# Optimization experiments

Measured on AMD Instinct MI355X. Metric: run time of the kernel, lower is better.

Reference implementation:

```python
import jax, jax.numpy as jnp
import numpy as np

N = 100000
E = 1600000
IN_DIM = 128
OUT_DIM = 128


def setup_inputs() -> dict:
    key = jax.random.key(0)
    k1, k2, k3, k4, k5 = jax.random.split(key, 5)
    x = jax.random.normal(k1, (N, IN_DIM), dtype=jnp.float32)
    edge_index = jax.random.randint(k2, (2, E), 0, N, dtype=jnp.int64)
    # LayerNorm affine params
    ln_w = jnp.ones((IN_DIM,), dtype=jnp.float32)
    ln_b = jnp.zeros((IN_DIM,), dtype=jnp.float32)
    # SAGEConv params: lin_l (neighbor agg, with bias), lin_r (root, no bias)
    s = 1.0 / np.sqrt(IN_DIM)
    W_l = jax.random.uniform(k3, (OUT_DIM, IN_DIM), dtype=jnp.float32, minval=-s, maxval=s)
    b_l = jax.random.uniform(k4, (OUT_DIM,), dtype=jnp.float32, minval=-s, maxval=s)
    W_r = jax.random.uniform(k5, (OUT_DIM, IN_DIM), dtype=jnp.float32, minval=-s, maxval=s)
    return {"x": x, "edge_index": edge_index, "ln_w": ln_w, "ln_b": ln_b,
            "W_l": W_l, "b_l": b_l, "W_r": W_r}


def _layer_norm(x, w, b, eps=1e-5):
    mu = jnp.mean(x, axis=-1, keepdims=True)
    var = jnp.mean(jnp.square(x - mu), axis=-1, keepdims=True)
    return (x - mu) * jax.lax.rsqrt(var + eps) * w + b


def reference(x, edge_index, ln_w, ln_b, W_l, b_l, W_r):
    # norm -> activation -> dropout(p=0, identity)
    h = jax.nn.relu(_layer_norm(x, ln_w, ln_b))  # [N, in_dim]
    src = edge_index[0]  # message sources (x_j)
    dst = edge_index[1]  # aggregation targets
    # mean aggregation of neighbor features onto target nodes
    agg = jax.ops.segment_sum(h[src], dst, num_segments=N)  # [N, in_dim]
    cnt = jax.ops.segment_sum(jnp.ones((E,), dtype=h.dtype), dst, num_segments=N)
    agg = agg / jnp.maximum(cnt, 1.0)[:, None]
    # SAGEConv: lin_l(agg) + lin_r(h)
    out = agg @ W_l.T + b_l + h @ W_r.T  # [N, out_dim]
    return out
```

## Files before the change

kernel.cpp:

```cpp
#include <hip/hip_runtime.h>

#define N_NODES 100000
#define E_EDGES 1600000
#define DIM     128

#define NB1     391
#define NBINS   512
#define NBH     (NBINS * NB1)
#define HS_BLOCKS 196

#define HB_OFF    0
#define WTB_OFF   25600000
#define OFFS_OFF  25665536
#define BH_OFF    26065600
#define BSUM_OFF  26868416
#define BIN_OFF   26869440
#define SRC_OFF   33269440

typedef __attribute__((ext_vector_type(8))) short short8;
typedef __attribute__((ext_vector_type(4))) float floatx4;

__device__ __forceinline__ unsigned bf16pack(float a, float b) {
  unsigned ua = __float_as_uint(a); ua += 0x7fffu + ((ua >> 16) & 1u);
  unsigned ub = __float_as_uint(b); ub += 0x7fffu + ((ub >> 16) & 1u);
  return (ua >> 16) | (ub & 0xffff0000u);
}
__device__ __forceinline__ float2 bf16unpack(unsigned p) {
  return make_float2(__uint_as_float(p << 16), __uint_as_float(p & 0xffff0000u));
}

__global__ __launch_bounds__(256) void k_prep(const float* __restrict__ x,
                                              const float* __restrict__ lw,
                                              const float* __restrict__ lb,
                                              const float* __restrict__ Wl,
                                              const float* __restrict__ Wr,
                                              const int* __restrict__ ei,
                                              unsigned* __restrict__ hb,
                                              unsigned* __restrict__ wtb,
                                              int* __restrict__ bh) {
  int gid = blockIdx.x * 256 + threadIdx.x;
  int t = threadIdx.x;

  {
    int row  = blockIdx.x * 4 + (t >> 6);
    int lane = t & 63;
    float2 v = ((const float2*)(x + (size_t)row * DIM))[lane];
    float s  = v.x + v.y;
    float sq = v.x * v.x + v.y * v.y;
    #pragma unroll
    for (int off = 32; off > 0; off >>= 1) {
      s  += __shfl_xor(s, off);
      sq += __shfl_xor(sq, off);
    }
    float mu  = s * (1.0f / 128.0f);
    float var = sq * (1.0f / 128.0f) - mu * mu;
    float rs  = rsqrtf(var + 1e-5f);
    float2 w = ((const float2*)lw)[lane];
    float2 b = ((const float2*)lb)[lane];
    float ox = fmaxf((v.x - mu) * rs * w.x + b.x, 0.0f);
    float oy = fmaxf((v.y - mu) * rs * w.y + b.y, 0.0f);
    hb[(size_t)row * 64 + lane] = bf16pack(ox, oy);
  }

  if (gid < 16384) {
    int j2 = gid & 3;
    int q  = (gid >> 2) & 3;
    int c  = (gid >> 4) & 127;
    int kb = gid >> 11;
    int k0 = kb * 32 + q * 8 + j2 * 2;
    int k1 = k0 + 1;
    float v0 = (k0 < 128) ? Wl[c * 128 + k0] : Wr[c * 128 + (k0 - 128)];
    float v1 = (k1 < 128) ? Wl[c * 128 + k1] : Wr[c * 128 + (k1 - 128)];
    wtb[gid] = bf16pack(v0, v1);
  }

  if (blockIdx.x < NB1) {
    __shared__ int h[NBINS];
    h[t] = 0; h[t + 256] = 0;
    __syncthreads();
    const int4* d4p = (const int4*)(ei + E_EDGES);
    #pragma unroll
    for (int u = 0; u < 4; ++u) {
      int i4 = blockIdx.x * 1024 + u * 256 + t;
      if (i4 < E_EDGES / 4) {
        int4 d = d4p[i4];
        atomicAdd(&h[d.x >> 8], 1);
        atomicAdd(&h[d.y >> 8], 1);
        atomicAdd(&h[d.z >> 8], 1);
        atomicAdd(&h[d.w >> 8], 1);
      }
    }
    __syncthreads();
    bh[t * NB1 + blockIdx.x] = h[t];
    bh[(t + 256) * NB1 + blockIdx.x] = h[t + 256];
  }
}

__global__ __launch_bounds__(256) void k_hscan1(int* __restrict__ bh,
                                                int* __restrict__ bsum) {
  __shared__ int s[256];
  int t = threadIdx.x;
  int base = blockIdx.x * 1024 + t * 4;
  int a0 = (base + 0 < NBH) ? bh[base + 0] : 0;
  int a1 = (base + 1 < NBH) ? bh[base + 1] : 0;
  int a2 = (base + 2 < NBH) ? bh[base + 2] : 0;
  int a3 = (base + 3 < NBH) ? bh[base + 3] : 0;
  s[t] = a0 + a1 + a2 + a3;
  __syncthreads();
  #pragma unroll
  for (int off = 1; off < 256; off <<= 1) {
    int x = (t >= off) ? s[t - off] : 0;
    __syncthreads();
    s[t] += x;
    __syncthreads();
  }
  int excl = (t > 0) ? s[t - 1] : 0;
  if (t == 255) bsum[blockIdx.x] = s[255];
  if (base + 0 < NBH) bh[base + 0] = excl;
  if (base + 1 < NBH) bh[base + 1] = excl + a0;
  if (base + 2 < NBH) bh[base + 2] = excl + a0 + a1;
  if (base + 3 < NBH) bh[base + 3] = excl + a0 + a1 + a2;
}

__global__ __launch_bounds__(256) void k_hscan2(int* __restrict__ bh,
                                                const int* __restrict__ bsum) {
  __shared__ int s[256];
  int t = threadIdx.x;
  s[t] = (t < HS_BLOCKS) ? bsum[t] : 0;
  __syncthreads();
  #pragma unroll
  for (int off = 1; off < 256; off <<= 1) {
    int x = (t >= off) ? s[t - off] : 0;
    __syncthreads();
    s[t] += x;
    __syncthreads();
  }
  int blk = blockIdx.x;
  int add = (blk > 0) ? s[blk - 1] : 0;
  #pragma unroll
  for (int u = 0; u < 4; ++u) {
    int i = blk * 1024 + t * 4 + u;
    if (i < NBH) bh[i] += add;
  }
}

__global__ __launch_bounds__(256) void k_scatter1(const int* __restrict__ ei,
                                                  const int* __restrict__ bh,
                                                  int* __restrict__ binned) {
  __shared__ int cur[NBINS];
  int t = threadIdx.x;
  cur[t] = bh[t * NB1 + blockIdx.x];
  cur[t + 256] = bh[(t + 256) * NB1 + blockIdx.x];
  __syncthreads();
  const int4* s4p = (const int4*)ei;
  const int4* d4p = (const int4*)(ei + E_EDGES);
  #pragma unroll
  for (int u = 0; u < 4; ++u) {
    int i4 = blockIdx.x * 1024 + u * 256 + t;
    if (i4 < E_EDGES / 4) {
      int4 sv = s4p[i4];
      int4 dv = d4p[i4];
      int p0 = atomicAdd(&cur[dv.x >> 8], 1);
      int p1 = atomicAdd(&cur[dv.y >> 8], 1);
      int p2 = atomicAdd(&cur[dv.z >> 8], 1);
      int p3 = atomicAdd(&cur[dv.w >> 8], 1);
      binned[p0] = sv.x | ((dv.x & 255) << 20);
      binned[p1] = sv.y | ((dv.y & 255) << 20);
      binned[p2] = sv.z | ((dv.z & 255) << 20);
      binned[p3] = sv.w | ((dv.w & 255) << 20);
    }
  }
}

__global__ __launch_bounds__(256) void k_csr(const int* __restrict__ bh,
                                             const int* __restrict__ binned,
                                             int* __restrict__ offs,
                                             int* __restrict__ srcidx) {
  __shared__ int h[256];
  __shared__ int s[256];
  __shared__ int cur[256];
  int t = threadIdx.x;
  int bin = blockIdx.x;
  int base = bh[bin * NB1];
  int end  = bh[(bin + 1) * NB1];
  h[t] = 0;
  __syncthreads();
  for (int i = base + t; i < end; i += 256)
    atomicAdd(&h[(binned[i] >> 20) & 255], 1);
  __syncthreads();
  s[t] = h[t];
  __syncthreads();
  #pragma unroll
  for (int off = 1; off < 256; off <<= 1) {
    int x = (t >= off) ? s[t - off] : 0;
    __syncthreads();
    s[t] += x;
    __syncthreads();
  }
  int excl = (t > 0) ? s[t - 1] : 0;
  cur[t] = excl;
  int node = bin * 256 + t;
  if (node < N_NODES) offs[node] = base + excl;
  if (node == N_NODES) offs[N_NODES] = E_EDGES;
  __syncthreads();
  for (int i = base + t; i < end; i += 256) {
    int p = binned[i];
    int r = atomicAdd(&cur[(p >> 20) & 255], 1);
    srcidx[base + r] = p & 0xFFFFF;
  }
}

__global__ __launch_bounds__(512) void k_gathgemm(const unsigned* __restrict__ hb,
                                                  const int* __restrict__ offs,
                                                  const int* __restrict__ srcidx,
                                                  const unsigned* __restrict__ wtb,
                                                  const float* __restrict__ bl,
                                                  float* __restrict__ out) {
  __shared__ unsigned agg[16 * 68];
  int wv   = threadIdx.x >> 6;
  int lane = threadIdx.x & 63;
  int r0 = blockIdx.x * 16;
  int n0 = r0 + wv * 2;
  int n1 = n0 + 1;
  int b0 = __builtin_amdgcn_readfirstlane(offs[n0]);
  int e0 = __builtin_amdgcn_readfirstlane(offs[n0 + 1]);
  int b1 = __builtin_amdgcn_readfirstlane(offs[n1]);
  int e1 = __builtin_amdgcn_readfirstlane(offs[n1 + 1]);
  int m0 = e0 - b0, m1 = e1 - b1;
  int c  = (m0 < m1 ? m0 : m1) & ~7;

  float ax0 = 0.0f, ay0 = 0.0f, ax1 = 0.0f, ay1 = 0.0f;

  for (int j = 0; j < c; j += 8) {
    unsigned p0[8], p1[8];
    #pragma unroll
    for (int i = 0; i < 8; ++i) {
      int s0 = srcidx[b0 + j + i];
      int s1 = srcidx[b1 + j + i];
      p0[i] = hb[(size_t)s0 * 64 + lane];
      p1[i] = hb[(size_t)s1 * 64 + lane];
    }
    #pragma unroll
    for (int i = 0; i < 8; ++i) {
      float2 v0 = bf16unpack(p0[i]);
      float2 v1 = bf16unpack(p1[i]);
      ax0 += v0.x; ay0 += v0.y;
      ax1 += v1.x; ay1 += v1.y;
    }
  }
  for (int j = b0 + c; j < e0; ) {
    int rem = e0 - j;
    if (rem >= 8) {
      unsigned p[8];
      #pragma unroll
      for (int i = 0; i < 8; ++i) p[i] = hb[(size_t)srcidx[j + i] * 64 + lane];
      #pragma unroll
      for (int i = 0; i < 8; ++i) { float2 v = bf16unpack(p[i]); ax0 += v.x; ay0 += v.y; }
      j += 8;
    } else {
      float2 v = bf16unpack(hb[(size_t)srcidx[j] * 64 + lane]);
      ax0 += v.x; ay0 += v.y;
      ++j;
    }
  }
  for (int j = b1 + c; j < e1; ) {
    int rem = e1 - j;
    if (rem >= 8) {
      unsigned p[8];
      #pragma unroll
      for (int i = 0; i < 8; ++i) p[i] = hb[(size_t)srcidx[j + i] * 64 + lane];
      #pragma unroll
      for (int i = 0; i < 8; ++i) { float2 v = bf16unpack(p[i]); ax1 += v.x; ay1 += v.y; }
      j += 8;
    } else {
      float2 v = bf16unpack(hb[(size_t)srcidx[j] * 64 + lane]);
      ax1 += v.x; ay1 += v.y;
      ++j;
    }
  }

  float inv0 = 1.0f / fmaxf((float)m0, 1.0f);
  float inv1 = 1.0f / fmaxf((float)m1, 1.0f);
  agg[(wv * 2 + 0) * 68 + lane] = bf16pack(ax0 * inv0, ay0 * inv0);
  agg[(wv * 2 + 1) * 68 + lane] = bf16pack(ax1 * inv1, ay1 * inv1);
  __syncthreads();

  int m = lane & 15;
  int q = lane >> 4;
  int rowA = r0 + m;

  short8 afrag[8];
  #pragma unroll
  for (int kb = 0; kb < 4; ++kb) {
    uint4 u = *(const uint4*)&agg[m * 68 + (kb * 4 + q) * 4];
    afrag[kb] = *(short8*)&u;
  }
  const uint4* hr = (const uint4*)(hb + (size_t)rowA * 64);
  #pragma unroll
  for (int kb = 0; kb < 4; ++kb) {
    uint4 u = hr[kb * 4 + q];
    afrag[kb + 4] = *(short8*)&u;
  }

  const uint4* b4 = (const uint4*)wtb;
  int ct = wv;
  int col = ct * 16 + m;
  floatx4 acc = {0.0f, 0.0f, 0.0f, 0.0f};
  #pragma unroll
  for (int kb = 0; kb < 8; ++kb) {
    uint4 u = b4[kb * 512 + col * 4 + q];
    short8 bfrag = *(short8*)&u;
    acc = __builtin_amdgcn_mfma_f32_16x16x32_bf16(afrag[kb], bfrag, acc, 0, 0, 0);
  }
  float bias = bl[col];
  #pragma unroll
  for (int reg = 0; reg < 4; ++reg) {
    int r = r0 + q * 4 + reg;
    out[(size_t)r * DIM + col] = acc[reg] + bias;
  }
}

extern "C" void kernel_launch(void* const* d_in, const int* in_sizes, int n_in,
                              void* d_out, int out_size, void* d_ws, size_t ws_size,
                              hipStream_t stream) {
  const float* x  = (const float*)d_in[0];
  const int*   ei = (const int*)d_in[1];
  const float* lw = (const float*)d_in[2];
  const float* lb = (const float*)d_in[3];
  const float* Wl = (const float*)d_in[4];
  const float* bl = (const float*)d_in[5];
  const float* Wr = (const float*)d_in[6];
  float* out = (float*)d_out;

  char* ws = (char*)d_ws;
  unsigned* hb     = (unsigned*)(ws + HB_OFF);
  unsigned* wtb    = (unsigned*)(ws + WTB_OFF);
  int*      offs   = (int*)(ws + OFFS_OFF);
  int*      bh     = (int*)(ws + BH_OFF);
  int*      bsum   = (int*)(ws + BSUM_OFF);
  int*      binned = (int*)(ws + BIN_OFF);
  int*      srcidx = (int*)(ws + SRC_OFF);

  k_prep<<<N_NODES / 4, 256, 0, stream>>>(x, lw, lb, Wl, Wr, ei, hb, wtb, bh);
  k_hscan1<<<HS_BLOCKS, 256, 0, stream>>>(bh, bsum);
  k_hscan2<<<HS_BLOCKS, 256, 0, stream>>>(bh, bsum);
  k_scatter1<<<NB1, 256, 0, stream>>>(ei, bh, binned);
  k_csr<<<NB1, 256, 0, stream>>>(bh, binned, offs, srcidx);
  k_gathgemm<<<N_NODES / 16, 512, 0, stream>>>(hb, offs, srcidx, wtb, bl, out);
}
```

Measured before the change: 261.7 us.

## Stage edge binning in shared memory before coalesced scatter to global

The bin-scatter kernel now processes 8192-edge chunks per block. Each block builds a local histogram and scan, places the packed edges into a shared-memory staging buffer ordered by bin, and then writes them out linearly, so global stores from each bin land in contiguous runs instead of random addresses. The chunk size doubles, which halves the number of per-block histogram columns and scan blocks, and the CSR launch count is decoupled from the chunk count. The cost is an extra histogram pass, about 64KB of LDS per block, and fewer blocks, which may lower occupancy.

```diff
diff --git a/kernel.cpp b/kernel.cpp
--- a/kernel.cpp
+++ b/kernel.cpp
@@ -4,18 +4,20 @@
 #define E_EDGES 1600000
 #define DIM     128
 
-#define NB1     391
+#define NB1     196
+#define CHUNK   8192
 #define NBINS   512
+#define NBUCKET 391
 #define NBH     (NBINS * NB1)
-#define HS_BLOCKS 196
+#define HS_BLOCKS 98
 
 #define HB_OFF    0
 #define WTB_OFF   25600000
 #define OFFS_OFF  25665536
 #define BH_OFF    26065600
-#define BSUM_OFF  26868416
-#define BIN_OFF   26869440
-#define SRC_OFF   33269440
+#define BSUM_OFF  26467008
+#define BIN_OFF   26468032
+#define SRC_OFF   32868032
 
 typedef __attribute__((ext_vector_type(8))) short short8;
 typedef __attribute__((ext_vector_type(4))) float floatx4;
@@ -80,8 +82,8 @@
     __syncthreads();
     const int4* d4p = (const int4*)(ei + E_EDGES);
     #pragma unroll
-    for (int u = 0; u < 4; ++u) {
-      int i4 = blockIdx.x * 1024 + u * 256 + t;
+    for (int u = 0; u < 8; ++u) {
+      int i4 = blockIdx.x * (CHUNK / 4) + u * 256 + t;
       if (i4 < E_EDGES / 4) {
         int4 d = d4p[i4];
         atomicAdd(&h[d.x >> 8], 1);
@@ -144,32 +146,92 @@
   }
 }
 
-__global__ __launch_bounds__(256) void k_scatter1(const int* __restrict__ ei,
-                                                  const int* __restrict__ bh,
-                                                  int* __restrict__ binned) {
+__global__ __launch_bounds__(256) void k_binsort(const int* __restrict__ ei,
+                                                 const int* __restrict__ bh,
+                                                 int* __restrict__ binned) {
+  __shared__ int stage[CHUNK];
+  __shared__ int addr[CHUNK];
+  __shared__ int hist[NBINS];
+  __shared__ int ebase[NBINS];
   __shared__ int cur[NBINS];
-  int t = threadIdx.x;
-  cur[t] = bh[t * NB1 + blockIdx.x];
-  cur[t + 256] = bh[(t + 256) * NB1 + blockIdx.x];
-  __syncthreads();
+  __shared__ int gbase[NBINS];
+  __shared__ int s[256];
+  int t  = threadIdx.x;
+  int ch = blockIdx.x;
+
+  hist[t] = 0; hist[t + 256] = 0;
+  gbase[t] = bh[t * NB1 + ch];
+  gbase[t + 256] = bh[(t + 256) * NB1 + ch];
+  __syncthreads();
+
   const int4* s4p = (const int4*)ei;
   const int4* d4p = (const int4*)(ei + E_EDGES);
-  #pragma unroll
-  for (int u = 0; u < 4; ++u) {
-    int i4 = blockIdx.x * 1024 + u * 256 + t;
+
+  #pragma unroll
+  for (int u = 0; u < 8; ++u) {
+    int i4 = ch * (CHUNK / 4) + u * 256 + t;
+    if (i4 < E_EDGES / 4) {
+      int4 d = d4p[i4];
+      atomicAdd(&hist[d.x >> 8], 1);
+      atomicAdd(&hist[d.y >> 8], 1);
+      atomicAdd(&hist[d.z >> 8], 1);
+      atomicAdd(&hist[d.w >> 8], 1);
+    }
+  }
+  __syncthreads();
+
+  int h0 = hist[2 * t], h1 = hist[2 * t + 1];
+  s[t] = h0 + h1;
+  __syncthreads();
+  #pragma unroll
+  for (int off = 1; off < 256; off <<= 1) {
+    int xv = (t >= off) ? s[t - off] : 0;
+    __syncthreads();
+    s[t] += xv;
+    __syncthreads();
+  }
+  int ex = (t > 0) ? s[t - 1] : 0;
+  ebase[2 * t] = ex;
+  ebase[2 * t + 1] = ex + h0;
+  cur[2 * t] = ex;
+  cur[2 * t + 1] = ex + h0;
+  __syncthreads();
+
+  #pragma unroll
+  for (int u = 0; u < 8; ++u) {
+    int i4 = ch * (CHUNK / 4) + u * 256 + t;
     if (i4 < E_EDGES / 4) {
       int4 sv = s4p[i4];
       int4 dv = d4p[i4];
-      int p0 = atomicAdd(&cur[dv.x >> 8], 1);
-      int p1 = atomicAdd(&cur[dv.y >> 8], 1);
-      int p2 = atomicAdd(&cur[dv.z >> 8], 1);
-      int p3 = atomicAdd(&cur[dv.w >> 8], 1);
-      binned[p0] = sv.x | ((dv.x & 255) << 20);
-      binned[p1] = sv.y | ((dv.y & 255) << 20);
-      binned[p2] = sv.z | ((dv.z & 255) << 20);
-      binned[p3] = sv.w | ((dv.w & 255) << 20);
-    }
-  }
+      {
+        int bin = dv.x >> 8; int pos = atomicAdd(&cur[bin], 1);
+        stage[pos] = sv.x | ((dv.x & 255) << 20);
+        addr[pos]  = gbase[bin] + (pos - ebase[bin]);
+      }
+      {
+        int bin = dv.y >> 8; int pos = atomicAdd(&cur[bin], 1);
+        stage[pos] = sv.y | ((dv.y & 255) << 20);
+        addr[pos]  = gbase[bin] + (pos - ebase[bin]);
+      }
+      {
+        int bin = dv.z >> 8; int pos = atomicAdd(&cur[bin], 1);
+        stage[pos] = sv.z | ((dv.z & 255) << 20);
+        addr[pos]  = gbase[bin] + (pos - ebase[bin]);
+      }
+      {
+        int bin = dv.w >> 8; int pos = atomicAdd(&cur[bin], 1);
+        stage[pos] = sv.w | ((dv.w & 255) << 20);
+        addr[pos]  = gbase[bin] + (pos - ebase[bin]);
+      }
+    }
+  }
+  __syncthreads();
+
+  int cbase = ch * CHUNK;
+  int cnt = E_EDGES - cbase;
+  if (cnt > CHUNK) cnt = CHUNK;
+  for (int i = t; i < cnt; i += 256)
+    binned[addr[i]] = stage[i];
 }
 
 __global__ __launch_bounds__(256) void k_csr(const int* __restrict__ bh,
@@ -303,8 +365,7 @@
   }
 
   const uint4* b4 = (const uint4*)wtb;
-  int ct = wv;
-  int col = ct * 16 + m;
+  int col = wv * 16 + m;
   floatx4 acc = {0.0f, 0.0f, 0.0f, 0.0f};
   #pragma unroll
   for (int kb = 0; kb < 8; ++kb) {
@@ -344,7 +405,7 @@
   k_prep<<<N_NODES / 4, 256, 0, stream>>>(x, lw, lb, Wl, Wr, ei, hb, wtb, bh);
   k_hscan1<<<HS_BLOCKS, 256, 0, stream>>>(bh, bsum);
   k_hscan2<<<HS_BLOCKS, 256, 0, stream>>>(bh, bsum);
-  k_scatter1<<<NB1, 256, 0, stream>>>(ei, bh, binned);
-  k_csr<<<NB1, 256, 0, stream>>>(bh, binned, offs, srcidx);
+  k_binsort<<<NB1, 256, 0, stream>>>(ei, bh, binned);
+  k_csr<<<NBUCKET, 256, 0, stream>>>(bh, binned, offs, srcidx);
   k_gathgemm<<<N_NODES / 16, 512, 0, stream>>>(hb, offs, srcidx, wtb, bl, out);
 }
```

Measured after the change: 254.4 us. 1.03x faster.
